# Kernel optimization log

Measured on AMD Instinct MI355X. Metric: run time of the kernel, lower is better.

## Reference

```python
import jax, jax.numpy as jnp
import numpy as np

N = 50000
E = 1600000
D_IN = 128
D_OUT = 128


def setup_inputs() -> dict:
    key = jax.random.key(0)
    k1, k2, k3, k4, k5 = jax.random.split(key, 5)
    feature = jax.random.normal(k1, (N, D_IN), dtype=jnp.float32)
    src = jax.random.randint(k2, (E,), 0, N, dtype=jnp.int32)
    dst = jax.random.randint(k3, (E,), 0, N, dtype=jnp.int32)
    # nn.Linear(in_feats, out_feats): weight [out, in], bias [out]
    bound = 1.0 / np.sqrt(D_IN)
    weight = jax.random.uniform(k4, (D_OUT, D_IN), minval=-bound, maxval=bound, dtype=jnp.float32)
    bias = jax.random.uniform(k5, (D_OUT,), minval=-bound, maxval=bound, dtype=jnp.float32)
    return {"feature": feature, "src": src, "dst": dst, "weight": weight, "bias": bias}


def reference(feature, src, dst, weight, bias):
    # message: copy src node feature along each edge; reduce: mean over incoming edges
    msgs = feature[src]                              # [E, D_IN] irregular gather
    summed = jax.ops.segment_sum(msgs, dst, num_segments=N)          # [N, D_IN]
    deg = jax.ops.segment_sum(jnp.ones((E,), dtype=feature.dtype), dst, num_segments=N)  # [N]
    # DGL update_all: zero-in-degree nodes keep their original 'h' (feature)
    mean = summed / jnp.maximum(deg, 1.0)[:, None]
    h = jnp.where((deg > 0)[:, None], mean, feature)  # [N, D_IN]
    out = h @ weight.T + bias                          # Linear
    return jax.nn.relu(out)
```

## Files before the change

kernel.cpp:

```cpp
#include <hip/hip_runtime.h>


#define NN 50000
#define EE 1600000
#define DD 128
#define NSTRIP 3125
#define GSB 782
#define SCAP 3072
#define CH3 4096
#define NW3 391
#define NFB3 1563

typedef __attribute__((ext_vector_type(8))) short bf16x8;
typedef __attribute__((ext_vector_type(8))) unsigned short u16x8;
typedef __attribute__((ext_vector_type(4))) float f32x4;

static __device__ __forceinline__ short f2bf(float f) {
  union { float f; unsigned u; } x; x.f = f;
  unsigned r = (x.u + 0x7FFF + ((x.u >> 16) & 1)) >> 16;
  return (short)(r & 0xFFFF);
}

__global__ __launch_bounds__(1024) void k3(
    const int* __restrict__ src, const int* __restrict__ dst,
    int* __restrict__ gcur, unsigned int* __restrict__ ss,
    const float* __restrict__ feature, unsigned short* __restrict__ fb) {
  if (blockIdx.x < NW3) {
    __shared__ int cnt[GSB];
    __shared__ int curb[GSB];
    const int base = blockIdx.x * CH3;
    for (int i = threadIdx.x; i < GSB; i += 1024) cnt[i] = 0;
    __syncthreads();

    {
      int e0 = base + threadIdx.x * 4;
      if (e0 < EE) {
        int4 d4 = *(const int4*)(dst + e0);
        atomicAdd(&cnt[((unsigned)d4.x) >> 6], 1);
        atomicAdd(&cnt[((unsigned)d4.y) >> 6], 1);
        atomicAdd(&cnt[((unsigned)d4.z) >> 6], 1);
        atomicAdd(&cnt[((unsigned)d4.w) >> 6], 1);
      }
    }
    __syncthreads();

    for (int i = threadIdx.x; i < GSB; i += 1024) {
      int c = cnt[i];
      int b = (c > 0) ? atomicAdd(&gcur[i * 16], c) : 0;
      curb[i] = i * SCAP + b;
    }
    __syncthreads();

    {
      int e0 = base + threadIdx.x * 4;
      if (e0 < EE) {
        int4 s4 = *(const int4*)(src + e0);
        int4 d4 = *(const int4*)(dst + e0);
        {
          int p = atomicAdd(&curb[((unsigned)d4.x) >> 6], 1);
          ss[p] = (((unsigned)d4.x) << 16) | (unsigned)s4.x;
        }
        {
          int p = atomicAdd(&curb[((unsigned)d4.y) >> 6], 1);
          ss[p] = (((unsigned)d4.y) << 16) | (unsigned)s4.y;
        }
        {
          int p = atomicAdd(&curb[((unsigned)d4.z) >> 6], 1);
          ss[p] = (((unsigned)d4.z) << 16) | (unsigned)s4.z;
        }
        {
          int p = atomicAdd(&curb[((unsigned)d4.w) >> 6], 1);
          ss[p] = (((unsigned)d4.w) << 16) | (unsigned)s4.w;
        }
      }
    }
  } else {
    int i = (blockIdx.x - NW3) * 1024 + threadIdx.x;
    if (i < NN * DD / 4) {
      float4 v = ((const float4*)feature)[i];
      short4 o;
      o.x = f2bf(v.x); o.y = f2bf(v.y); o.z = f2bf(v.z); o.w = f2bf(v.w);
      ((short4*)fb)[i] = o;
    }
  }
}

__global__ __launch_bounds__(1024) void fillagg(
    const unsigned int* __restrict__ ss, const int* __restrict__ gcur,
    const unsigned short* __restrict__ fb,
    unsigned short* __restrict__ hb) {
  __shared__ int win[SCAP];
  __shared__ int cur[64];
  __shared__ int rs[65];
  const int g  = blockIdx.x;
  const int lo = g * 64;
  const int nl = (NN - lo < 64) ? (NN - lo) : 64;
  const int ebase = g * SCAP;
  const int eend  = ebase + gcur[g * 16];

  if (threadIdx.x < 64) cur[threadIdx.x] = 0;
  __syncthreads();
  for (int e = ebase + threadIdx.x; e < eend; e += 1024) {
    atomicAdd(&cur[(ss[e] >> 16) & 63], 1);
  }
  __syncthreads();

  if (threadIdx.x < 64) {
    const int lane = threadIdx.x;
    int v = cur[lane];
    int x = v;
#pragma unroll
    for (int d = 1; d < 64; d <<= 1) { int t = __shfl_up(x, d, 64); if (lane >= d) x += t; }
    rs[lane + 1] = x;
    if (lane == 0) rs[0] = 0;
    cur[lane] = 0;
  }
  __syncthreads();

  for (int e = ebase + threadIdx.x; e < eend; e += 1024) {
    unsigned pe = ss[e];
    int li = (pe >> 16) & 63;
    int p = atomicAdd(&cur[li], 1);
    win[rs[li] + p] = (int)(pe & 0xFFFFu);
  }
  __syncthreads();

  const int wv = threadIdx.x >> 6;
  const int lane = threadIdx.x & 63;
  const int q  = lane >> 4;
  const int sl = lane & 15;
  const u16x8* fp = (const u16x8*)fb;

  for (int ln = wv; ln < nl; ln += 16) {
    const int st = rs[ln];
    const int en = rs[ln + 1];
    const int deg = en - st;
    const int n = lo + ln;

    float acc[8];
#pragma unroll
    for (int j = 0; j < 8; ++j) acc[j] = 0.f;

#pragma unroll 4
    for (int e = st + q; e < en; e += 4) {
      int s = win[e];
      u16x8 v = fp[(size_t)s * 16 + sl];
#pragma unroll
      for (int j = 0; j < 8; ++j) {
        union { unsigned u; float f; } c; c.u = ((unsigned)v[j]) << 16;
        acc[j] += c.f;
      }
    }
#pragma unroll
    for (int j = 0; j < 8; ++j) {
      acc[j] += __shfl_xor(acc[j], 16, 64);
      acc[j] += __shfl_xor(acc[j], 32, 64);
    }

    if (q == 0) {
      u16x8 hv;
      if (deg > 0) {
        float inv = 1.0f / (float)deg;
#pragma unroll
        for (int j = 0; j < 8; ++j) hv[j] = (unsigned short)f2bf(acc[j] * inv);
      } else {
        hv = fp[(size_t)n * 16 + sl];
      }
      ((u16x8*)hb)[(size_t)n * 16 + sl] = hv;
    }
  }
}

__global__ __launch_bounds__(256) void mfma_gemm2(
    const short* __restrict__ hb,
    const float* __restrict__ weight,
    const float* __restrict__ bias,
    float* __restrict__ out) {
  __shared__ bf16x8 wfrag[2048];
  __shared__ float  bias_l[DD];

#pragma unroll
  for (int k = 0; k < 8; ++k) {
    int idx  = threadIdx.x * 8 + k;
    int ln   = idx & 63;
    int ct   = idx >> 6;
    int c    = ct >> 2;
    int t    = ct & 3;
    const float* wp = weight + (c * 16 + (ln & 15)) * DD + t * 32 + (ln >> 4) * 8;
    float4 w0 = *(const float4*)(wp);
    float4 w1 = *(const float4*)(wp + 4);
    bf16x8 b;
    b[0] = f2bf(w0.x); b[1] = f2bf(w0.y); b[2] = f2bf(w0.z); b[3] = f2bf(w0.w);
    b[4] = f2bf(w1.x); b[5] = f2bf(w1.y); b[6] = f2bf(w1.z); b[7] = f2bf(w1.w);
    wfrag[idx] = b;
  }
  if (threadIdx.x < DD) bias_l[threadIdx.x] = bias[threadIdx.x];
  __syncthreads();

  const int wave = threadIdx.x >> 6;
  const int lane = threadIdx.x & 63;
  const int r  = lane & 15;
  const int g  = lane >> 4;

#pragma unroll
  for (int s = 0; s < 2; ++s) {
    const int strip = blockIdx.x * 8 + wave * 2 + s;
    if (strip >= NSTRIP) continue;
    const int m0 = strip * 16;

    bf16x8 Af[4];
#pragma unroll
    for (int t = 0; t < 4; ++t) {
      Af[t] = *(const bf16x8*)(hb + (size_t)(m0 + r) * DD + t * 32 + g * 8);
    }

#pragma unroll
    for (int c = 0; c < 8; ++c) {
      f32x4 acc = {0.f, 0.f, 0.f, 0.f};
#pragma unroll
      for (int t = 0; t < 4; ++t) {
        acc = __builtin_amdgcn_mfma_f32_16x16x32_bf16(Af[t], wfrag[(c * 4 + t) * 64 + lane], acc, 0, 0, 0);
      }
      const float b = bias_l[c * 16 + r];
#pragma unroll
      for (int q = 0; q < 4; ++q) {
        int row = m0 + g * 4 + q;
        float v = acc[q] + b;
        out[(size_t)row * DD + c * 16 + r] = v > 0.f ? v : 0.f;
      }
    }
  }
}

extern "C" void kernel_launch(void* const* d_in, const int* in_sizes, int n_in,
                              void* d_out, int out_size, void* d_ws, size_t ws_size,
                              hipStream_t stream) {
  const float* feature = (const float*)d_in[0];
  const int*   src     = (const int*)d_in[1];
  const int*   dst     = (const int*)d_in[2];
  const float* weight  = (const float*)d_in[3];
  const float* bias    = (const float*)d_in[4];
  float* out = (float*)d_out;

  int* gcur = (int*)d_ws;
  unsigned short* hb = (unsigned short*)(gcur + 12512);

  unsigned int* ss = (unsigned int*)d_out;
  unsigned short* fb = (unsigned short*)((int*)d_out + GSB * SCAP);

  (void)hipMemsetAsync(gcur, 0, 12512 * sizeof(int), stream);

  k3<<<NW3 + NFB3, 1024, 0, stream>>>(src, dst, gcur, ss, feature, fb);
  fillagg<<<GSB, 1024, 0, stream>>>(ss, gcur, fb, hb);
  mfma_gemm2<<<(NSTRIP + 7) / 8, 256, 0, stream>>>((const short*)hb, weight, bias, out);
}
```

Before: 105.3 us.

## Split bf16 feature table into four column panels and gather per panel

```diff
diff --git a/kernel.cpp b/kernel.cpp
--- a/kernel.cpp
+++ b/kernel.cpp
@@ -9,7 +9,7 @@
 #define SCAP 3072
 #define CH3 4096
 #define NW3 391
-#define NFB3 1563
+#define NFB3 782
 
 typedef __attribute__((ext_vector_type(8))) short bf16x8;
 typedef __attribute__((ext_vector_type(8))) unsigned short u16x8;
@@ -75,12 +75,18 @@
       }
     }
   } else {
-    int i = (blockIdx.x - NW3) * 1024 + threadIdx.x;
-    if (i < NN * DD / 4) {
-      float4 v = ((const float4*)feature)[i];
-      short4 o;
-      o.x = f2bf(v.x); o.y = f2bf(v.y); o.z = f2bf(v.z); o.w = f2bf(v.w);
-      ((short4*)fb)[i] = o;
+    int u = (blockIdx.x - NW3) * 1024 + threadIdx.x;
+    if (u < NN * 16) {
+      int n = u >> 4;
+      int s = u & 15;
+      float4 v0 = ((const float4*)feature)[u * 2];
+      float4 v1 = ((const float4*)feature)[u * 2 + 1];
+      u16x8 o;
+      o[0] = (unsigned short)f2bf(v0.x); o[1] = (unsigned short)f2bf(v0.y);
+      o[2] = (unsigned short)f2bf(v0.z); o[3] = (unsigned short)f2bf(v0.w);
+      o[4] = (unsigned short)f2bf(v1.x); o[5] = (unsigned short)f2bf(v1.y);
+      o[6] = (unsigned short)f2bf(v1.z); o[7] = (unsigned short)f2bf(v1.w);
+      ((u16x8*)fb)[((size_t)(s >> 2) * NN + n) * 4 + (s & 3)] = o;
     }
   }
 }
@@ -127,8 +133,8 @@
 
   const int wv = threadIdx.x >> 6;
   const int lane = threadIdx.x & 63;
-  const int q  = lane >> 4;
-  const int sl = lane & 15;
+  const int eq = lane >> 2;
+  const int j4 = lane & 3;
   const u16x8* fp = (const u16x8*)fb;
 
   for (int ln = wv; ln < nl; ln += 16) {
@@ -137,36 +143,41 @@
     const int deg = en - st;
     const int n = lo + ln;
 
-    float acc[8];
-#pragma unroll
-    for (int j = 0; j < 8; ++j) acc[j] = 0.f;
-
-#pragma unroll 4
-    for (int e = st + q; e < en; e += 4) {
-      int s = win[e];
-      u16x8 v = fp[(size_t)s * 16 + sl];
+#pragma unroll
+    for (int p = 0; p < 4; ++p) {
+      float acc[8];
+#pragma unroll
+      for (int j = 0; j < 8; ++j) acc[j] = 0.f;
+
+#pragma unroll 2
+      for (int e = st + eq; e < en; e += 16) {
+        int s = win[e];
+        u16x8 v = fp[((size_t)p * NN + s) * 4 + j4];
+#pragma unroll
+        for (int j = 0; j < 8; ++j) {
+          union { unsigned u; float f; } c; c.u = ((unsigned)v[j]) << 16;
+          acc[j] += c.f;
+        }
+      }
 #pragma unroll
       for (int j = 0; j < 8; ++j) {
-        union { unsigned u; float f; } c; c.u = ((unsigned)v[j]) << 16;
-        acc[j] += c.f;
-      }
-    }
-#pragma unroll
-    for (int j = 0; j < 8; ++j) {
-      acc[j] += __shfl_xor(acc[j], 16, 64);
-      acc[j] += __shfl_xor(acc[j], 32, 64);
-    }
-
-    if (q == 0) {
-      u16x8 hv;
-      if (deg > 0) {
-        float inv = 1.0f / (float)deg;
-#pragma unroll
-        for (int j = 0; j < 8; ++j) hv[j] = (unsigned short)f2bf(acc[j] * inv);
-      } else {
-        hv = fp[(size_t)n * 16 + sl];
-      }
-      ((u16x8*)hb)[(size_t)n * 16 + sl] = hv;
+        acc[j] += __shfl_xor(acc[j], 4, 64);
+        acc[j] += __shfl_xor(acc[j], 8, 64);
+        acc[j] += __shfl_xor(acc[j], 16, 64);
+        acc[j] += __shfl_xor(acc[j], 32, 64);
+      }
+
+      if (eq == 0) {
+        u16x8 hv;
+        if (deg > 0) {
+          float inv = 1.0f / (float)deg;
+#pragma unroll
+          for (int j = 0; j < 8; ++j) hv[j] = (unsigned short)f2bf(acc[j] * inv);
+        } else {
+          hv = fp[((size_t)p * NN + n) * 4 + j4];
+        }
+        ((u16x8*)hb)[(size_t)n * 16 + p * 4 + j4] = hv;
+      }
     }
   }
 }
```

Result: slower. 158.6 us (+50.6%).
